# Optimization experiments

Measured on AMD Instinct MI355X. Metric: run time of the kernel, lower is better.

The kernel has to match this reference:

```python
import jax, jax.numpy as jnp
import numpy as np

BT = 80        # B*T frames (B=8, T=10)
MAX_N = 13     # cfg.num_boxes
K2D = 26400    # K*K*D = 5*5*1056 (crop_size^2 * emb_features)
NFB = 1024     # cfg.num_features_boxes
A = 6          # cfg.num_actions
G = 5          # cfg.num_activities


def setup_inputs() -> dict:
    key = jax.random.key(0)
    k = jax.random.split(key, 8)
    # RoIAlign box features, already flattened per box: [BT, MAX_N, K*K*D]
    boxes_features_flat = jax.random.normal(k[0], (BT, MAX_N, K2D), jnp.float32)
    # ragged per-frame box counts in [1, MAX_N]
    bboxes_num = jax.random.randint(k[1], (BT,), 1, MAX_N + 1, dtype=jnp.int32)
    # kaiming-normal linear weights (fan_in scaling), zero biases (per nn.Linear default bias ~0 scale)
    w_emb = jax.random.normal(k[2], (K2D, NFB), jnp.float32) * np.float32(np.sqrt(2.0 / K2D))
    b_emb = jnp.zeros((NFB,), jnp.float32)
    w_act = jax.random.normal(k[3], (NFB, A), jnp.float32) * np.float32(np.sqrt(2.0 / NFB))
    b_act = jnp.zeros((A,), jnp.float32)
    w_acty = jax.random.normal(k[4], (NFB, G), jnp.float32) * np.float32(np.sqrt(2.0 / NFB))
    b_acty = jnp.zeros((G,), jnp.float32)
    return {
        "boxes_features_flat": boxes_features_flat,
        "w_emb": w_emb, "b_emb": b_emb,
        "w_act": w_act, "b_act": b_act,
        "w_acty": w_acty, "b_acty": b_acty,
        "bboxes_num": bboxes_num,
    }


def reference(boxes_features_flat, w_emb, b_emb, w_act, b_act, w_acty, b_acty, bboxes_num):
    # fc_emb_1 + ReLU (dropout is identity at inference)
    h = jax.nn.relu(jnp.einsum('bnk,kf->bnf', boxes_features_flat, w_emb) + b_emb)  # [BT, MAX_N, NFB]
    # validity mask replacing the per-frame ragged slice boxes_features_all[bt, :N]
    mask = jnp.arange(MAX_N)[None, :] < bboxes_num[:, None]  # [BT, MAX_N]
    # per-box action scores; invalid (padded) boxes zeroed
    actions_scores = (jnp.einsum('bnf,fa->bna', h, w_act) + b_act) * mask[..., None].astype(h.dtype)
    # masked max-pool over valid boxes per frame (N >= 1 always)
    neg = jnp.finfo(h.dtype).min
    pooled = jnp.max(jnp.where(mask[..., None], h, neg), axis=1)  # [BT, NFB]
    activities_scores = pooled @ w_acty + b_acty  # [BT, G]
    return actions_scores, activities_scores
```

## Files before the change

### kernel.cpp

```cpp
#include <hip/hip_runtime.h>

#define K2D 26400
#define NFB 1024
#define NBT 80
#define MAXN 13
#define MTOT (NBT * MAXN)
#define NA 6
#define NG 5
#define KITERS 825
#define TILEB 8192
#define AIMG 10
#define NT128 8
#define MT256 5
#define NT256 4
#define ITS 5
#define ITG (KITERS / ITS)

typedef __attribute__((ext_vector_type(8))) short     bf16x8;
typedef __attribute__((ext_vector_type(4))) float     f32x4;
typedef __attribute__((ext_vector_type(4))) unsigned short us4;
typedef __attribute__((ext_vector_type(8))) unsigned short us8;

__device__ __forceinline__ unsigned short f2bf(float x) {
    unsigned u = __float_as_uint(x);
    u += 0x7fffu + ((u >> 16) & 1u);
    return (unsigned short)(u >> 16);
}

__device__ __forceinline__ void gload_lds16(const void* g, void* l) {
    __builtin_amdgcn_global_load_lds(
        (const __attribute__((address_space(1))) unsigned int*)g,
        (__attribute__((address_space(3))) unsigned int*)l, 16, 0, 0);
}

#define META_OFFS 1
#define META_MAP  82

__global__ __launch_bounds__(256) void prefix_kernel(const int* __restrict__ nb,
                                                     int* __restrict__ meta)
{
    __shared__ int a[128];
    const int t = threadIdx.x;
    if (t < 128) a[t] = (t < NBT) ? nb[t] : 0;
    __syncthreads();
#pragma unroll
    for (int s = 1; s < 128; s <<= 1) {
        int v = 0;
        if (t < 128 && t >= s) v = a[t - s];
        __syncthreads();
        if (t < 128) a[t] += v;
        __syncthreads();
    }
    if (t == 0) { meta[0] = a[NBT - 1]; meta[META_OFFS] = 0; }
    if (t < NBT) meta[META_OFFS + t + 1] = a[t];
    for (int f = t; f < NBT * MAXN; f += 256) {
        const int bt = f / MAXN, n = f % MAXN;
        const int o0 = bt ? a[bt - 1] : 0;
        if (n < a[bt] - o0) meta[META_MAP + o0 + n] = f;
    }
}

__global__ __launch_bounds__(256, 4) void pack_ab(
    const float* __restrict__ A, const float* __restrict__ W,
    const int* __restrict__ meta,
    unsigned short* __restrict__ Aout, unsigned short* __restrict__ Bout)
{
    const int id = blockIdx.x, t = threadIdx.x;

    if (id < KITERS) {
        const int it = id;
        const float* wbase = W + (size_t)it * 32 * NFB;
        unsigned short* ob = Bout + (size_t)it * (TILEB / 2);
#pragma unroll
        for (int cp = 0; cp < 8; ++cp) {
            const int c0 = (2 * cp) * 256 + t;
            const int c1 = c0 + 256;
            const int bn0 = c0 >> 9, q0 = (c0 >> 7) & 3, n0 = c0 & 127;
            const int bn1 = c1 >> 9, q1 = (c1 >> 7) & 3, n1 = c1 & 127;
            const float* bp0 = wbase + (size_t)(q0 * 8) * NFB + bn0 * 128 + n0;
            const float* bp1 = wbase + (size_t)(q1 * 8) * NFB + bn1 * 128 + n1;
            float v0[8], v1[8];
#pragma unroll
            for (int j = 0; j < 8; ++j) v0[j] = bp0[(size_t)j * NFB];
#pragma unroll
            for (int j = 0; j < 8; ++j) v1[j] = bp1[(size_t)j * NFB];
            us8 u0, u1;
#pragma unroll
            for (int j = 0; j < 8; ++j) u0[j] = f2bf(v0[j]);
#pragma unroll
            for (int j = 0; j < 8; ++j) u1[j] = f2bf(v1[j]);
            *(us8*)(ob + (size_t)bn0 * KITERS * (TILEB / 2) + (q0 * 128 + n0) * 8) = u0;
            *(us8*)(ob + (size_t)bn1 * KITERS * (TILEB / 2) + (q1 * 128 + n1) * 8) = u1;
        }
        return;
    }

    const int id2 = id - KITERS;
    const int bm  = id2 / ITG;
    const int itg = id2 % ITG;
    const int total = meta[0];
    if (bm * 128 >= total) return;
    const int it0 = itg * ITS;
#pragma unroll
    for (int i = 0; i < 4; ++i) {
        const int f  = t + i * 256;
        const int m  = f >> 3;
        const int kp = (f & 7) * 4;
        const int p  = bm * 128 + m;
        const int src = (p < total) ? meta[META_MAP + p] : 0;
        const float* ap = A + (size_t)src * K2D + it0 * 32 + kp;
        unsigned short* ob = Aout + (size_t)(bm * KITERS + it0) * (TILEB / 2)
                           + (kp >> 3) * 1024 + m * 8 + (kp & 7);
        float4 v[ITS];
#pragma unroll
        for (int j = 0; j < ITS; ++j) {
            float4 w = {0.f, 0.f, 0.f, 0.f};
            if (p < total) w = *(const float4*)(ap + j * 32);
            v[j] = w;
        }
#pragma unroll
        for (int j = 0; j < ITS; ++j) {
            us4 u = { f2bf(v[j].x), f2bf(v[j].y), f2bf(v[j].z), f2bf(v[j].w) };
            *(us4*)(ob + (size_t)j * (TILEB / 2)) = u;
        }
    }
}

__global__ __launch_bounds__(512, 2) void gemm_pipe(
    const unsigned short* __restrict__ Apack,
    const unsigned short* __restrict__ Bpack,
    float* __restrict__ Cp,
    const int* __restrict__ meta, int kchunk)
{
    __shared__ __attribute__((aligned(16))) unsigned short buf[3][4][4][128][8];

    const int id     = (int)blockIdx.x;
    const int npairs = (int)(gridDim.x >> 2);
    const int nmain  = npairs & ~7;
    int pair, bn;
    if (id < (nmain << 2)) { pair = ((id >> 5) << 3) + (id & 7); bn = (id >> 3) & 3; }
    else { const int r = id - (nmain << 2); pair = nmain + (r >> 2); bn = r & 3; }
    const int nch = npairs / MT256;
    const int bm  = pair / nch;
    const int s   = pair % nch;

    const int total = meta[0];
    if (bm * 256 >= total) return;

    const int t = threadIdx.x;
    const int wave = t >> 6, lane = t & 63;
    const int quad = lane >> 4, l16 = lane & 15;
    const int wmq = wave & 3;
    const int asel = wmq >> 1;
    const int wm128 = (wmq & 1) * 64;
    const int bsel = wave >> 2;
    const int it0 = s * kchunk;
    const int it1 = min(KITERS, it0 + kchunk);

    f32x4 acc[4][8] = {};

    {
        const int itlast = it1 - 1;
        const char* A0 = (const char*)Apack + (size_t)(2 * bm) * KITERS * TILEB;
        const char* A1 = (const char*)Apack + (size_t)(2 * bm + 1) * KITERS * TILEB;
        const char* B0 = (const char*)Bpack + (size_t)(2 * bn) * KITERS * TILEB;
        const char* B1 = (const char*)Bpack + (size_t)(2 * bn + 1) * KITERS * TILEB;
        const int go = t * 16;
        const int lo = wave * 1024;

#define ISSUE(IT, ST) do {                                                     \
    const size_t o_ = (size_t)(IT) * TILEB;                                    \
    gload_lds16(A0 + o_ + go, (char*)&buf[ST][0] + lo);                        \
    gload_lds16(A1 + o_ + go, (char*)&buf[ST][1] + lo);                        \
    gload_lds16(B0 + o_ + go, (char*)&buf[ST][2] + lo);                        \
    gload_lds16(B1 + o_ + go, (char*)&buf[ST][3] + lo);                        \
} while (0)

        ISSUE(it0, 0);
        { const int itp = min(it0 + 1, itlast); ISSUE(itp, 1); }

#define STEP(ITV, CUR, DST) do {                                               \
    asm volatile("" ::: "memory");                                             \
    __builtin_amdgcn_s_waitcnt(0xF74);                           \
    __builtin_amdgcn_s_barrier();                                              \
    asm volatile("" ::: "memory");                                             \
    int itn = (ITV) + 2; itn = itn > itlast ? itlast : itn;                    \
    ISSUE(itn, DST);                                                           \
    bf16x8 af[4], bfr[8];                                                      \
    _Pragma("unroll")                                                          \
    for (int x = 0; x < 4; ++x)                                                \
        af[x] = *(const bf16x8*)(&buf[CUR][asel][quad][wm128 + x * 16 + l16][0]); \
    _Pragma("unroll")                                                          \
    for (int y = 0; y < 8; ++y)                                                \
        bfr[y] = *(const bf16x8*)(&buf[CUR][2 + bsel][quad][y * 16 + l16][0]); \
    _Pragma("unroll")                                                          \
    for (int x = 0; x < 4; ++x)                                                \
        _Pragma("unroll")                                                      \
        for (int y = 0; y < 8; ++y)                                            \
            acc[x][y] = __builtin_amdgcn_mfma_f32_16x16x32_bf16(               \
                af[x], bfr[y], acc[x][y], 0, 0, 0);                            \
} while (0)

        for (int it = it0; it < it1; it += 3) {
            STEP(it,     0, 2);
            STEP(it + 1, 1, 0);
            STEP(it + 2, 2, 1);
        }
#undef STEP
#undef ISSUE
    }

#pragma unroll
    for (int x = 0; x < 4; ++x) {
        const int rowb = bm * 256 + wmq * 64 + x * 16 + quad * 4;
#pragma unroll
        for (int y = 0; y < 8; ++y) {
            const int col = bn * 256 + bsel * 128 + y * 16 + l16;
#pragma unroll
            for (int r = 0; r < 4; ++r) {
                const int rr = rowb + r;
                if (rr < MTOT)
                    Cp[((size_t)s * MTOT + rr) * NFB + col] = acc[x][y][r];
            }
        }
    }
}

__global__ __launch_bounds__(256) void reduce_kernel(
    const float* __restrict__ Cp, const float* __restrict__ b_emb,
    float* __restrict__ h, const int* __restrict__ meta, int splitk)
{
    const int row = blockIdx.x;
    if (row >= meta[0]) return;
    const int t = threadIdx.x;
    const size_t base = (size_t)row * NFB + t * 4;
    float4 v = *(const float4*)(Cp + base);
#pragma unroll 4
    for (int s2 = 1; s2 < splitk; ++s2) {
        const float4 w = *(const float4*)(Cp + (size_t)s2 * MTOT * NFB + base);
        v.x += w.x; v.y += w.y; v.z += w.z; v.w += w.w;
    }
    const float4 be = *(const float4*)(b_emb + t * 4);
    v.x = fmaxf(v.x + be.x, 0.f);
    v.y = fmaxf(v.y + be.y, 0.f);
    v.z = fmaxf(v.z + be.z, 0.f);
    v.w = fmaxf(v.w + be.w, 0.f);
    *(float4*)(h + base) = v;
}

__global__ __launch_bounds__(256) void heads_kernel(
    const float* __restrict__ h,
    const float* __restrict__ w_act,  const float* __restrict__ b_act,
    const float* __restrict__ w_acty, const float* __restrict__ b_acty,
    const int* __restrict__ meta, float* __restrict__ out)
{
    __shared__ __attribute__((aligned(16))) float hs[MAXN][NFB];
    __shared__ float pooled[NFB];
    const int bt = blockIdx.x;
    const int t  = threadIdx.x;
    const int off0 = meta[META_OFFS + bt];
    const int Nb   = meta[META_OFFS + bt + 1] - off0;

    for (int i = 0; i < MAXN; ++i)
        if (i < Nb)
            *(float4*)(&hs[i][t * 4]) =
                *(const float4*)(h + (size_t)(off0 + i) * NFB + t * 4);
    __syncthreads();

    const int wave = t >> 6, lane = t & 63;

    for (int d = wave; d < MAXN * NA; d += 4) {
        const int n = d / NA, a = d % NA;
        if (n < Nb) {
            float sum = 0.f;
            for (int f = lane; f < NFB; f += 64)
                sum += hs[n][f] * w_act[f * NA + a];
#pragma unroll
            for (int o = 32; o > 0; o >>= 1) sum += __shfl_xor(sum, o);
            if (lane == 0) out[bt * (MAXN * NA) + d] = sum + b_act[a];
        } else {
            if (lane == 0) out[bt * (MAXN * NA) + d] = 0.f;
        }
    }

    for (int f = t; f < NFB; f += 256) {
        float m = hs[0][f];
        for (int n2 = 1; n2 < Nb; ++n2) m = fmaxf(m, hs[n2][f]);
        pooled[f] = m;
    }
    __syncthreads();

    for (int g = wave; g < NG; g += 4) {
        float sum = 0.f;
        for (int f = lane; f < NFB; f += 64)
            sum += pooled[f] * w_acty[f * NG + g];
#pragma unroll
        for (int o = 32; o > 0; o >>= 1) sum += __shfl_xor(sum, o);
        if (lane == 0)
            out[NBT * MAXN * NA + bt * NG + g] = sum + b_acty[g];
    }
}

__global__ __launch_bounds__(256) void gemm_f32(
    const float* __restrict__ A, const float* __restrict__ B,
    float* __restrict__ Cp, int kchunk)
{
    __shared__ __attribute__((aligned(16))) unsigned short Alds[4][128][8];
    __shared__ __attribute__((aligned(16))) unsigned short Blds[4][128][8];
    const int t = threadIdx.x;
    const int bm = blockIdx.x, bn = blockIdx.y, s = blockIdx.z;
    const int wave = t >> 6, lane = t & 63;
    const int quad = lane >> 4, l16 = lane & 15;
    const int wm = (wave & 1) * 64, wn = (wave >> 1) * 64;
    const int row0 = bm * 128, col0 = bn * 128;
    const int it0 = s * kchunk, it1 = min(KITERS, it0 + kchunk);

    f32x4 acc[4][4] = {};
    for (int it = it0; it < it1; ++it) {
        const int k0 = it * 32;
#pragma unroll
        for (int i = 0; i < 4; ++i) {
            const int f = t + i * 256, m = f >> 3, kp = (f & 7) * 4;
            const int gr = row0 + m;
            float4 v = {0.f, 0.f, 0.f, 0.f};
            if (gr < MTOT) v = *(const float4*)(A + (size_t)gr * K2D + k0 + kp);
            us4 u = { f2bf(v.x), f2bf(v.y), f2bf(v.z), f2bf(v.w) };
            *(us4*)(&Alds[kp >> 3][m][kp & 7]) = u;
        }
#pragma unroll
        for (int i = 0; i < 2; ++i) {
            const int p = t + i * 256, n = p & 127, kq = p >> 7;
            const float* bp = B + (size_t)(k0 + kq * 8) * NFB + (col0 + n);
            us8 u;
#pragma unroll
            for (int j = 0; j < 8; ++j) u[j] = f2bf(bp[(size_t)j * NFB]);
            *(us8*)(&Blds[kq][n][0]) = u;
        }
        __syncthreads();
        bf16x8 af[4], bfr[4];
#pragma unroll
        for (int x = 0; x < 4; ++x) {
            af[x]  = *(const bf16x8*)(&Alds[quad][wm + x * 16 + l16][0]);
            bfr[x] = *(const bf16x8*)(&Blds[quad][wn + x * 16 + l16][0]);
        }
#pragma unroll
        for (int x = 0; x < 4; ++x)
#pragma unroll
            for (int y = 0; y < 4; ++y)
                acc[x][y] = __builtin_amdgcn_mfma_f32_16x16x32_bf16(
                    af[x], bfr[y], acc[x][y], 0, 0, 0);
        __syncthreads();
    }
#pragma unroll
    for (int x = 0; x < 4; ++x) {
        const int rowb = row0 + wm + x * 16 + quad * 4;
#pragma unroll
        for (int y = 0; y < 4; ++y) {
            const int col = col0 + wn + y * 16 + l16;
#pragma unroll
            for (int r = 0; r < 4; ++r) {
                const int rr = rowb + r;
                if (rr < MTOT)
                    Cp[((size_t)s * MTOT + rr) * NFB + col] = acc[x][y][r];
            }
        }
    }
}

__global__ __launch_bounds__(256) void finalize_fallback(
    const float* __restrict__ Cp, const float* __restrict__ b_emb,
    const float* __restrict__ w_act, const float* __restrict__ b_act,
    const float* __restrict__ w_acty, const float* __restrict__ b_acty,
    const int* __restrict__ bboxes_num, float* __restrict__ out, int splitk)
{
    __shared__ __attribute__((aligned(16))) float h[MAXN][NFB];
    __shared__ float pooled[NFB];
    const int bt = blockIdx.x;
    const int t  = threadIdx.x;
    const int Nb = bboxes_num[bt];

    for (int i = 0; i < MAXN; ++i) {
        const int flat = i * 256 + t;
        const int row  = flat >> 8;
        const int f4   = flat & 255;
        const size_t base = ((size_t)(bt * MAXN + row)) * NFB + f4 * 4;
        float4 v = *(const float4*)(Cp + base);
        for (int s2 = 1; s2 < splitk; ++s2) {
            const float4 w = *(const float4*)(Cp + (size_t)s2 * MTOT * NFB + base);
            v.x += w.x; v.y += w.y; v.z += w.z; v.w += w.w;
        }
        const float4 be = *(const float4*)(b_emb + f4 * 4);
        v.x = fmaxf(v.x + be.x, 0.f);
        v.y = fmaxf(v.y + be.y, 0.f);
        v.z = fmaxf(v.z + be.z, 0.f);
        v.w = fmaxf(v.w + be.w, 0.f);
        *(float4*)(&h[row][f4 * 4]) = v;
    }
    __syncthreads();
    const int wave = t >> 6, lane = t & 63;
    for (int d = wave; d < MAXN * NA; d += 4) {
        const int n = d / NA, a = d % NA;
        float sum = 0.f;
        for (int f = lane; f < NFB; f += 64)
            sum += h[n][f] * w_act[f * NA + a];
#pragma unroll
        for (int o = 32; o > 0; o >>= 1) sum += __shfl_xor(sum, o);
        if (lane == 0)
            out[bt * (MAXN * NA) + d] = (n < Nb) ? (sum + b_act[a]) : 0.f;
    }
    for (int f = t; f < NFB; f += 256) {
        float m = h[0][f];
        for (int n2 = 1; n2 < Nb; ++n2) m = fmaxf(m, h[n2][f]);
        pooled[f] = m;
    }
    __syncthreads();
    for (int g = wave; g < NG; g += 4) {
        float sum = 0.f;
        for (int f = lane; f < NFB; f += 64)
            sum += pooled[f] * w_acty[f * NG + g];
#pragma unroll
        for (int o = 32; o > 0; o >>= 1) sum += __shfl_xor(sum, o);
        if (lane == 0)
            out[NBT * MAXN * NA + bt * NG + g] = sum + b_acty[g];
    }
}

extern "C" void kernel_launch(void* const* d_in, const int* in_sizes, int n_in,
                              void* d_out, int out_size, void* d_ws, size_t ws_size,
                              hipStream_t stream) {
    const float* A      = (const float*)d_in[0];
    const float* W      = (const float*)d_in[1];
    const float* b_emb  = (const float*)d_in[2];
    const float* w_act  = (const float*)d_in[3];
    const float* b_act  = (const float*)d_in[4];
    const float* w_acty = (const float*)d_in[5];
    const float* b_acty = (const float*)d_in[6];
    const int*   bboxes = (const int*)d_in[7];
    float* out = (float*)d_out;

    const size_t PACKA = (size_t)AIMG * KITERS * TILEB;
    const size_t PACKB = (size_t)NT128 * KITERS * TILEB;
    const size_t PART  = (size_t)MTOT * NFB * 4;
    const size_t METAB = 8192;

    long avail = (long)ws_size - (long)(PACKA + PACKB + METAB);
    int splitk = (int)(avail / (long)PART);
    if (splitk > 20) splitk = 20;

    if (splitk >= 4) {
        const int kchunk = ((KITERS + 3 * splitk - 1) / (3 * splitk)) * 3;
        const int nchunks = (KITERS + kchunk - 1) / kchunk;

        unsigned short* Ap = (unsigned short*)d_ws;
        unsigned short* Bp = (unsigned short*)((char*)d_ws + PACKA);
        float* Cp = (float*)((char*)d_ws + PACKA + PACKB);
        int* meta = (int*)((char*)d_ws + PACKA + PACKB + (size_t)splitk * PART);
        float* h  = (float*)d_ws;

        prefix_kernel<<<1, 256, 0, stream>>>(bboxes, meta);
        pack_ab<<<dim3(KITERS + AIMG * ITG), 256, 0, stream>>>(A, W, meta, Ap, Bp);
        gemm_pipe<<<dim3(NT256 * nchunks * MT256), 512, 0, stream>>>(Ap, Bp, Cp,
                                                                     meta, kchunk);
        reduce_kernel<<<MTOT, 256, 0, stream>>>(Cp, b_emb, h, meta, nchunks);
        heads_kernel<<<NBT, 256, 0, stream>>>(h, w_act, b_act, w_acty, b_acty,
                                              meta, out);
    } else {
        float* Cp = (float*)d_ws;
        gemm_f32<<<dim3(9, 8, 4), 256, 0, stream>>>(A, W, Cp, 207);
        finalize_fallback<<<NBT, 256, 0, stream>>>(Cp, b_emb, w_act, b_act,
                                                   w_acty, b_acty, bboxes, out, 4);
    }
}
```

Before: 354.3 us.

## Load fp32 activations directly into LDS in GEMM, drop separate A packing

Removes the A-side pack pass (gather of valid boxes plus bf16 conversion into a workspace) and instead has the GEMM kernel gather fp32 activation rows straight into LDS with async global-to-LDS loads, using an XOR swizzle. Conversion to bf16 happens in registers via packed cvt instructions before the MFMAs. This saves a full write and re-read of the packed A buffer and one kernel's worth of traffic, at the cost of doubled LDS footprint per stage (fp32 A tiles), more LDS reads, extra convert instructions in the inner loop, and possibly reduced occupancy. Freeing the workspace used by packed A also changes how much is available for split-K partials.

```diff
diff --git a/kernel.cpp b/kernel.cpp
--- a/kernel.cpp
+++ b/kernel.cpp
@@ -9,12 +9,9 @@
 #define NG 5
 #define KITERS 825
 #define TILEB 8192
-#define AIMG 10
 #define NT128 8
 #define MT256 5
 #define NT256 4
-#define ITS 5
-#define ITG (KITERS / ITS)
 
 typedef __attribute__((ext_vector_type(8))) short     bf16x8;
 typedef __attribute__((ext_vector_type(4))) float     f32x4;
@@ -31,6 +28,17 @@
     __builtin_amdgcn_global_load_lds(
         (const __attribute__((address_space(1))) unsigned int*)g,
         (__attribute__((address_space(3))) unsigned int*)l, 16, 0, 0);
+}
+
+__device__ __forceinline__ bf16x8 cvt8(f32x4 lo, f32x4 hi) {
+    unsigned r0, r1, r2, r3;
+    asm("v_cvt_pk_bf16_f32 %0, %1, %2" : "=v"(r0) : "v"(lo[0]), "v"(lo[1]));
+    asm("v_cvt_pk_bf16_f32 %0, %1, %2" : "=v"(r1) : "v"(lo[2]), "v"(lo[3]));
+    asm("v_cvt_pk_bf16_f32 %0, %1, %2" : "=v"(r2) : "v"(hi[0]), "v"(hi[1]));
+    asm("v_cvt_pk_bf16_f32 %0, %1, %2" : "=v"(r3) : "v"(hi[2]), "v"(hi[3]));
+    union { unsigned u[4]; bf16x8 v; } o;
+    o.u[0] = r0; o.u[1] = r1; o.u[2] = r2; o.u[3] = r3;
+    return o.v;
 }
 
 #define META_OFFS 1
@@ -60,79 +68,42 @@
     }
 }
 
-__global__ __launch_bounds__(256, 4) void pack_ab(
-    const float* __restrict__ A, const float* __restrict__ W,
-    const int* __restrict__ meta,
-    unsigned short* __restrict__ Aout, unsigned short* __restrict__ Bout)
-{
-    const int id = blockIdx.x, t = threadIdx.x;
-
-    if (id < KITERS) {
-        const int it = id;
-        const float* wbase = W + (size_t)it * 32 * NFB;
-        unsigned short* ob = Bout + (size_t)it * (TILEB / 2);
-#pragma unroll
-        for (int cp = 0; cp < 8; ++cp) {
-            const int c0 = (2 * cp) * 256 + t;
-            const int c1 = c0 + 256;
-            const int bn0 = c0 >> 9, q0 = (c0 >> 7) & 3, n0 = c0 & 127;
-            const int bn1 = c1 >> 9, q1 = (c1 >> 7) & 3, n1 = c1 & 127;
-            const float* bp0 = wbase + (size_t)(q0 * 8) * NFB + bn0 * 128 + n0;
-            const float* bp1 = wbase + (size_t)(q1 * 8) * NFB + bn1 * 128 + n1;
-            float v0[8], v1[8];
-#pragma unroll
-            for (int j = 0; j < 8; ++j) v0[j] = bp0[(size_t)j * NFB];
-#pragma unroll
-            for (int j = 0; j < 8; ++j) v1[j] = bp1[(size_t)j * NFB];
-            us8 u0, u1;
-#pragma unroll
-            for (int j = 0; j < 8; ++j) u0[j] = f2bf(v0[j]);
-#pragma unroll
-            for (int j = 0; j < 8; ++j) u1[j] = f2bf(v1[j]);
-            *(us8*)(ob + (size_t)bn0 * KITERS * (TILEB / 2) + (q0 * 128 + n0) * 8) = u0;
-            *(us8*)(ob + (size_t)bn1 * KITERS * (TILEB / 2) + (q1 * 128 + n1) * 8) = u1;
-        }
-        return;
-    }
-
-    const int id2 = id - KITERS;
-    const int bm  = id2 / ITG;
-    const int itg = id2 % ITG;
-    const int total = meta[0];
-    if (bm * 128 >= total) return;
-    const int it0 = itg * ITS;
-#pragma unroll
-    for (int i = 0; i < 4; ++i) {
-        const int f  = t + i * 256;
-        const int m  = f >> 3;
-        const int kp = (f & 7) * 4;
-        const int p  = bm * 128 + m;
-        const int src = (p < total) ? meta[META_MAP + p] : 0;
-        const float* ap = A + (size_t)src * K2D + it0 * 32 + kp;
-        unsigned short* ob = Aout + (size_t)(bm * KITERS + it0) * (TILEB / 2)
-                           + (kp >> 3) * 1024 + m * 8 + (kp & 7);
-        float4 v[ITS];
-#pragma unroll
-        for (int j = 0; j < ITS; ++j) {
-            float4 w = {0.f, 0.f, 0.f, 0.f};
-            if (p < total) w = *(const float4*)(ap + j * 32);
-            v[j] = w;
-        }
-#pragma unroll
-        for (int j = 0; j < ITS; ++j) {
-            us4 u = { f2bf(v[j].x), f2bf(v[j].y), f2bf(v[j].z), f2bf(v[j].w) };
-            *(us4*)(ob + (size_t)j * (TILEB / 2)) = u;
-        }
+__global__ __launch_bounds__(256, 4) void pack_b(
+    const float* __restrict__ W, unsigned short* __restrict__ Bout)
+{
+    const int it = blockIdx.x, t = threadIdx.x;
+    const float* wbase = W + (size_t)it * 32 * NFB;
+    unsigned short* ob = Bout + (size_t)it * (TILEB / 2);
+#pragma unroll
+    for (int cp = 0; cp < 8; ++cp) {
+        const int c0 = (2 * cp) * 256 + t;
+        const int c1 = c0 + 256;
+        const int bn0 = c0 >> 9, q0 = (c0 >> 7) & 3, n0 = c0 & 127;
+        const int bn1 = c1 >> 9, q1 = (c1 >> 7) & 3, n1 = c1 & 127;
+        const float* bp0 = wbase + (size_t)(q0 * 8) * NFB + bn0 * 128 + n0;
+        const float* bp1 = wbase + (size_t)(q1 * 8) * NFB + bn1 * 128 + n1;
+        float v0[8], v1[8];
+#pragma unroll
+        for (int j = 0; j < 8; ++j) v0[j] = bp0[(size_t)j * NFB];
+#pragma unroll
+        for (int j = 0; j < 8; ++j) v1[j] = bp1[(size_t)j * NFB];
+        us8 u0, u1;
+#pragma unroll
+        for (int j = 0; j < 8; ++j) u0[j] = f2bf(v0[j]);
+#pragma unroll
+        for (int j = 0; j < 8; ++j) u1[j] = f2bf(v1[j]);
+        *(us8*)(ob + (size_t)bn0 * KITERS * (TILEB / 2) + (q0 * 128 + n0) * 8) = u0;
+        *(us8*)(ob + (size_t)bn1 * KITERS * (TILEB / 2) + (q1 * 128 + n1) * 8) = u1;
     }
 }
 
 __global__ __launch_bounds__(512, 2) void gemm_pipe(
-    const unsigned short* __restrict__ Apack,
+    const float* __restrict__ A,
     const unsigned short* __restrict__ Bpack,
     float* __restrict__ Cp,
     const int* __restrict__ meta, int kchunk)
 {
-    __shared__ __attribute__((aligned(16))) unsigned short buf[3][4][4][128][8];
+    __shared__ __attribute__((aligned(16))) char smem[3][49152];
 
     const int id     = (int)blockIdx.x;
     const int npairs = (int)(gridDim.x >> 2);
@@ -151,29 +122,36 @@
     const int wave = t >> 6, lane = t & 63;
     const int quad = lane >> 4, l16 = lane & 15;
     const int wmq = wave & 3;
-    const int asel = wmq >> 1;
-    const int wm128 = (wmq & 1) * 64;
     const int bsel = wave >> 2;
     const int it0 = s * kchunk;
     const int it1 = min(KITERS, it0 + kchunk);
 
+    const float* baseA[4];
+#pragma unroll
+    for (int j = 0; j < 4; ++j) {
+        const int R = wave * 32 + j * 8 + (lane >> 3);
+        const int p = bm * 256 + R;
+        const int src = (p < total) ? meta[META_MAP + p] : 0;
+        const int segsw = (lane & 7) ^ ((lane >> 3) & 7);
+        baseA[j] = A + (size_t)src * K2D + segsw * 4;
+    }
+
     f32x4 acc[4][8] = {};
 
     {
         const int itlast = it1 - 1;
-        const char* A0 = (const char*)Apack + (size_t)(2 * bm) * KITERS * TILEB;
-        const char* A1 = (const char*)Apack + (size_t)(2 * bm + 1) * KITERS * TILEB;
         const char* B0 = (const char*)Bpack + (size_t)(2 * bn) * KITERS * TILEB;
         const char* B1 = (const char*)Bpack + (size_t)(2 * bn + 1) * KITERS * TILEB;
-        const int go = t * 16;
-        const int lo = wave * 1024;
 
 #define ISSUE(IT, ST) do {                                                     \
-    const size_t o_ = (size_t)(IT) * TILEB;                                    \
-    gload_lds16(A0 + o_ + go, (char*)&buf[ST][0] + lo);                        \
-    gload_lds16(A1 + o_ + go, (char*)&buf[ST][1] + lo);                        \
-    gload_lds16(B0 + o_ + go, (char*)&buf[ST][2] + lo);                        \
-    gload_lds16(B1 + o_ + go, (char*)&buf[ST][3] + lo);                        \
+    char* sa = &smem[ST][0] + wave * 4096;                                     \
+    _Pragma("unroll")                                                          \
+    for (int j = 0; j < 4; ++j)                                                \
+        gload_lds16(baseA[j] + (size_t)(IT) * 32, sa + j * 1024);              \
+    gload_lds16(B0 + (size_t)(IT) * TILEB + t * 16,                            \
+                &smem[ST][32768] + wave * 1024);                               \
+    gload_lds16(B1 + (size_t)(IT) * TILEB + t * 16,                            \
+                &smem[ST][40960] + wave * 1024);                               \
 } while (0)
 
         ISSUE(it0, 0);
@@ -181,18 +159,25 @@
 
 #define STEP(ITV, CUR, DST) do {                                               \
     asm volatile("" ::: "memory");                                             \
-    __builtin_amdgcn_s_waitcnt(0xF74);                           \
+    __builtin_amdgcn_s_waitcnt(0xF76);                           \
     __builtin_amdgcn_s_barrier();                                              \
     asm volatile("" ::: "memory");                                             \
     int itn = (ITV) + 2; itn = itn > itlast ? itlast : itn;                    \
     ISSUE(itn, DST);                                                           \
     bf16x8 af[4], bfr[8];                                                      \
     _Pragma("unroll")                                                          \
-    for (int x = 0; x < 4; ++x)                                                \
-        af[x] = *(const bf16x8*)(&buf[CUR][asel][quad][wm128 + x * 16 + l16][0]); \
+    for (int x = 0; x < 4; ++x) {                                              \
+        const int R = wmq * 64 + x * 16 + l16;                                 \
+        const char* ra = &smem[CUR][0] + R * 128;                              \
+        const int sw = l16 & 7;                                                \
+        f32x4 lo = *(const f32x4*)(ra + (((2 * quad)     ^ sw) * 16));         \
+        f32x4 hi = *(const f32x4*)(ra + (((2 * quad + 1) ^ sw) * 16));         \
+        af[x] = cvt8(lo, hi);                                                  \
+    }                                                                          \
     _Pragma("unroll")                                                          \
     for (int y = 0; y < 8; ++y)                                                \
-        bfr[y] = *(const bf16x8*)(&buf[CUR][2 + bsel][quad][y * 16 + l16][0]); \
+        bfr[y] = *(const bf16x8*)(&smem[CUR][32768] + bsel * 8192              \
+                                  + quad * 2048 + (y * 16 + l16) * 16);        \
     _Pragma("unroll")                                                          \
     for (int x = 0; x < 4; ++x)                                                \
         _Pragma("unroll")                                                      \
@@ -438,12 +423,11 @@
     const int*   bboxes = (const int*)d_in[7];
     float* out = (float*)d_out;
 
-    const size_t PACKA = (size_t)AIMG * KITERS * TILEB;
     const size_t PACKB = (size_t)NT128 * KITERS * TILEB;
     const size_t PART  = (size_t)MTOT * NFB * 4;
     const size_t METAB = 8192;
 
-    long avail = (long)ws_size - (long)(PACKA + PACKB + METAB);
+    long avail = (long)ws_size - (long)(PACKB + METAB);
     int splitk = (int)(avail / (long)PART);
     if (splitk > 20) splitk = 20;
 
@@ -451,15 +435,14 @@
         const int kchunk = ((KITERS + 3 * splitk - 1) / (3 * splitk)) * 3;
         const int nchunks = (KITERS + kchunk - 1) / kchunk;
 
-        unsigned short* Ap = (unsigned short*)d_ws;
-        unsigned short* Bp = (unsigned short*)((char*)d_ws + PACKA);
-        float* Cp = (float*)((char*)d_ws + PACKA + PACKB);
-        int* meta = (int*)((char*)d_ws + PACKA + PACKB + (size_t)splitk * PART);
+        unsigned short* Bp = (unsigned short*)d_ws;
+        float* Cp = (float*)((char*)d_ws + PACKB);
+        int* meta = (int*)((char*)d_ws + PACKB + (size_t)splitk * PART);
         float* h  = (float*)d_ws;
 
         prefix_kernel<<<1, 256, 0, stream>>>(bboxes, meta);
-        pack_ab<<<dim3(KITERS + AIMG * ITG), 256, 0, stream>>>(A, W, meta, Ap, Bp);
-        gemm_pipe<<<dim3(NT256 * nchunks * MT256), 512, 0, stream>>>(Ap, Bp, Cp,
+        pack_b<<<dim3(KITERS), 256, 0, stream>>>(W, Bp);
+        gemm_pipe<<<dim3(NT256 * nchunks * MT256), 512, 0, stream>>>(A, Bp, Cp,
                                                                      meta, kchunk);
         reduce_kernel<<<MTOT, 256, 0, stream>>>(Cp, b_emb, h, meta, nchunks);
         heads_kernel<<<NBT, 256, 0, stream>>>(h, w_act, b_act, w_acty, b_acty,
```

Measured after the change: 347.5 us. About the same (-1.9%).
